# Performance work log

Hardware: AMD Instinct MI355X
Metric: run time of the kernel (lower is better)

## Reference

```python
import jax, jax.numpy as jnp
import numpy as np

NUM_CLASSES = 81
THRESH_HI = 0.5
THRESH_LO = 0.4
GAMMA = 2.0
ALPHA = 0.25
VARIANCE = (0.1, 0.2)  # cfg['variance'] in ssd.pytorch
B, P, T = 32, 24564, 20


def setup_inputs() -> dict:
    key = jax.random.key(0)
    k1, k2, k3, k4, k5, k6, k7 = jax.random.split(key, 7)
    loc_data = jax.random.normal(k1, (B, P, 4), jnp.float32)
    conf_data = jax.random.normal(k2, (B, P, NUM_CLASSES), jnp.float32)
    # priors in center form (cx, cy, w, h), all in [0,1]
    pcxy = jax.random.uniform(k3, (P, 2), minval=0.05, maxval=0.95)
    pwh = jax.random.uniform(k4, (P, 2), minval=0.04, maxval=0.5)
    priors = jnp.concatenate([pcxy, pwh], axis=-1).astype(jnp.float32)
    # ground-truth boxes in point form (xmin, ymin, xmax, ymax) + label
    tcxy = jax.random.uniform(k5, (B, T, 2), minval=0.1, maxval=0.9)
    twh = jax.random.uniform(k6, (B, T, 2), minval=0.05, maxval=0.4)
    boxes = jnp.clip(jnp.concatenate([tcxy - twh / 2, tcxy + twh / 2], -1), 0.0, 1.0)
    labels = jax.random.randint(k7, (B, T), 0, NUM_CLASSES - 1).astype(jnp.float32)
    targets = jnp.concatenate([boxes, labels[..., None]], axis=-1)  # [B,T,5]
    return {"loc_data": loc_data, "conf_data": conf_data, "priors": priors, "targets": targets}


def point_form(pr):
    # center form -> (xmin,ymin,xmax,ymax)
    return jnp.concatenate([pr[:, :2] - pr[:, 2:] / 2, pr[:, :2] + pr[:, 2:] / 2], -1)


def jaccard(box_a, box_b):
    # box_a [T,4], box_b [P,4], both point form -> IoU [T,P]
    lt = jnp.maximum(box_a[:, None, :2], box_b[None, :, :2])
    rb = jnp.minimum(box_a[:, None, 2:], box_b[None, :, 2:])
    wh = jnp.clip(rb - lt, 0.0)
    inter = wh[..., 0] * wh[..., 1]
    area_a = ((box_a[:, 2] - box_a[:, 0]) * (box_a[:, 3] - box_a[:, 1]))[:, None]
    area_b = ((box_b[:, 2] - box_b[:, 0]) * (box_b[:, 3] - box_b[:, 1]))[None, :]
    return inter / (area_a + area_b - inter)


def encode(matched, priors):
    # matched [P,4] point form, priors [P,4] center form
    g_cxcy = ((matched[:, :2] + matched[:, 2:]) / 2 - priors[:, :2]) / (VARIANCE[0] * priors[:, 2:])
    g_wh = jnp.log((matched[:, 2:] - matched[:, :2]) / priors[:, 2:]) / VARIANCE[1]
    return jnp.concatenate([g_cxcy, g_wh], -1)


def match_one(truths, labels, priors):
    # truths [T,4] point form, labels [T], priors [P,4] center form
    ov = jaccard(truths, point_form(priors))          # [T,P]
    best_prior_idx = jnp.argmax(ov, axis=1)           # [T] best prior per gt
    best_truth_overlap = jnp.max(ov, axis=0)          # [P]
    best_truth_idx = jnp.argmax(ov, axis=0)           # [P]
    # ensure every gt box keeps its best prior
    best_truth_overlap = best_truth_overlap.at[best_prior_idx].set(2.0)
    best_truth_idx = best_truth_idx.at[best_prior_idx].set(jnp.arange(truths.shape[0]))
    matched = truths[best_truth_idx]                  # [P,4]
    conf = labels[best_truth_idx].astype(jnp.int32) + 1
    conf = jnp.where(best_truth_overlap < THRESH_HI, -1, conf)  # ignore band
    conf = jnp.where(best_truth_overlap < THRESH_LO, 0, conf)   # background
    return encode(matched, priors), conf


def reference(loc_data, conf_data, priors, targets):
    truths = targets[..., :4]
    labels = targets[..., 4]
    loc_t, conf_t = jax.vmap(lambda t, l: match_one(t, l, priors))(truths, labels)
    pos = conf_t > 0                                  # [B,P]
    # smooth L1 over positive priors (sum reduction)
    diff = loc_data - loc_t
    ad = jnp.abs(diff)
    sl1 = jnp.where(ad < 1.0, 0.5 * diff * diff, ad - 0.5)
    loss_l = jnp.sum(sl1 * pos[..., None])
    # focal loss over ALL locations (ignore conf==-1)
    logits = conf_data.reshape(-1, NUM_CLASSES)
    tgt = conf_t.reshape(-1)
    valid = tgt >= 0
    tgt_safe = jnp.where(valid, tgt, 0)
    logpt = jnp.take_along_axis(jax.nn.log_softmax(logits, -1), tgt_safe[:, None], 1)[:, 0]
    pt = jnp.exp(logpt)
    alpha_t = jnp.where(tgt > 0, ALPHA, 1.0 - ALPHA)
    fl = -alpha_t * (1.0 - pt) ** GAMMA * logpt
    loss_c = jnp.sum(jnp.where(valid, fl, 0.0))
    n = jnp.sum(pos).astype(loc_data.dtype)
    return loss_l / n, loss_c / n
```

## Files before the change

kernel.cpp:

```cpp
#include <hip/hip_runtime.h>

#define NCLS 81
#define BB 32
#define PP 24564
#define TT 20
#define KM_BLOCKS_X 96
#define BP_SEGS 8
#define BP_SEG 3072
#define KL_BLOCKS 1792
#define KL_ROWS 32
#define KL_CHUNKS ((BB * PP) / KL_ROWS)
#define KL_F4 ((KL_ROWS * NCLS) / 4)

#define GLOAD_LDS16(g, l)                                                  \
    __builtin_amdgcn_global_load_lds(                                      \
        (const __attribute__((address_space(1))) void*)(g),                \
        (__attribute__((address_space(3))) void*)(l), 16, 0, 0)

__global__ __launch_bounds__(1024)
void k_bp(const float* __restrict__ priors,
          const float* __restrict__ targets,
          unsigned long long* __restrict__ bp_part)
{
    const int seg = blockIdx.x;
    const int b = blockIdx.y;

    __shared__ float trb[TT * 5];
    __shared__ unsigned long long wred[TT][16];
    if (threadIdx.x < TT * 5) trb[threadIdx.x] = targets[b * TT * 5 + threadIdx.x];
    __syncthreads();

    float X1[3], Y1[3], X2[3], Y2[3], pa[3];
    unsigned int pkey[3];
    bool ok[3];
    #pragma unroll
    for (int j = 0; j < 3; ++j) {
        int p = seg * BP_SEG + j * 1024 + threadIdx.x;
        ok[j] = p < PP;
        float4 pr = ok[j] ? ((const float4*)priors)[p] : make_float4(1.f, 1.f, 0.f, 0.f);
        float hw = __fmul_rn(pr.z, 0.5f), hh = __fmul_rn(pr.w, 0.5f);
        X1[j] = __fsub_rn(pr.x, hw); Y1[j] = __fsub_rn(pr.y, hh);
        X2[j] = __fadd_rn(pr.x, hw); Y2[j] = __fadd_rn(pr.y, hh);
        pa[j] = __fmul_rn(__fsub_rn(X2[j], X1[j]), __fsub_rn(Y2[j], Y1[j]));
        pkey[j] = 0xFFFFFFFFu - (unsigned)p;
    }

    const int wv = threadIdx.x >> 6;
    const int lane = threadIdx.x & 63;

    for (int t = 0; t < TT; ++t) {
        float tx1 = trb[t * 5 + 0], ty1 = trb[t * 5 + 1];
        float tx2 = trb[t * 5 + 2], ty2 = trb[t * 5 + 3];
        float ta = __fmul_rn(__fsub_rn(tx2, tx1), __fsub_rn(ty2, ty1));

        unsigned long long best = 0ull;
        #pragma unroll
        for (int j = 0; j < 3; ++j) {
            float lx = fmaxf(tx1, X1[j]), ly = fmaxf(ty1, Y1[j]);
            float rx = fminf(tx2, X2[j]), ry = fminf(ty2, Y2[j]);
            float w = fmaxf(__fsub_rn(rx, lx), 0.0f);
            float h = fmaxf(__fsub_rn(ry, ly), 0.0f);
            float inter = __fmul_rn(w, h);
            float denom = __fsub_rn(__fadd_rn(ta, pa[j]), inter);
            float ov = __fdiv_rn(inter, denom);
            unsigned long long key = ok[j]
                ? (((unsigned long long)__float_as_uint(ov) << 32) | pkey[j]) : 0ull;
            if (key > best) best = key;
        }
        #pragma unroll
        for (int s = 32; s; s >>= 1) {
            unsigned long long o = __shfl_xor(best, s, 64);
            if (o > best) best = o;
        }
        if (lane == 0) wred[t][wv] = best;
    }
    __syncthreads();
    if (threadIdx.x < TT) {
        unsigned long long m = wred[threadIdx.x][0];
        #pragma unroll
        for (int w = 1; w < 16; ++w) if (wred[threadIdx.x][w] > m) m = wred[threadIdx.x][w];
        bp_part[(b * TT + threadIdx.x) * BP_SEGS + seg] = m;
    }
}

__global__ __launch_bounds__(256)
void k_match(const float* __restrict__ loc,
             const float* __restrict__ priors,
             const float* __restrict__ targets,
             const unsigned long long* __restrict__ bp_part,
             unsigned char* __restrict__ code,
             float* __restrict__ pl, float* __restrict__ pn)
{
    const int b = blockIdx.y;
    const int p = blockIdx.x * 256 + threadIdx.x;

    __shared__ float trb[TT * 5];
    __shared__ unsigned int bpb[TT];
    if (threadIdx.x < TT * 5) trb[threadIdx.x] = targets[b * TT * 5 + threadIdx.x];
    if (threadIdx.x < TT) {
        const unsigned long long* q = bp_part + (b * TT + threadIdx.x) * BP_SEGS;
        unsigned long long m = q[0];
        #pragma unroll
        for (int s = 1; s < BP_SEGS; ++s) if (q[s] > m) m = q[s];
        bpb[threadIdx.x] = 0xFFFFFFFFu - (unsigned)(m & 0xFFFFFFFFull);
    }
    __syncthreads();

    float accL = 0.0f, accN = 0.0f;

    if (p < PP) {
        float px = priors[p * 4 + 0], py = priors[p * 4 + 1];
        float pw = priors[p * 4 + 2], ph = priors[p * 4 + 3];
        float hw = __fmul_rn(pw, 0.5f), hh = __fmul_rn(ph, 0.5f);
        float X1 = __fsub_rn(px, hw), Y1 = __fsub_rn(py, hh);
        float X2 = __fadd_rn(px, hw), Y2 = __fadd_rn(py, hh);
        float pa = __fmul_rn(__fsub_rn(X2, X1), __fsub_rn(Y2, Y1));

        float bI = -1.0f, bD = 1.0f;
        int bt = 0;
        #pragma unroll
        for (int t = 0; t < TT; ++t) {
            float tx1 = trb[t * 5 + 0], ty1 = trb[t * 5 + 1];
            float tx2 = trb[t * 5 + 2], ty2 = trb[t * 5 + 3];
            float ta2 = __fmul_rn(__fsub_rn(tx2, tx1), __fsub_rn(ty2, ty1));
            float lx = fmaxf(tx1, X1), ly = fmaxf(ty1, Y1);
            float rx = fminf(tx2, X2), ry = fminf(ty2, Y2);
            float w = fmaxf(__fsub_rn(rx, lx), 0.0f);
            float h = fmaxf(__fsub_rn(ry, ly), 0.0f);
            float inter = __fmul_rn(w, h);
            float denom = __fsub_rn(__fadd_rn(ta2, pa), inter);
            if (__fmul_rn(inter, bD) > __fmul_rn(bI, denom)) { bI = inter; bD = denom; bt = t; }
        }
        float bov = __fdiv_rn(bI, bD);

        bool forced = false;
        #pragma unroll
        for (int t = 0; t < TT; ++t) {
            if (bpb[t] == (unsigned)p) { bt = t; forced = true; }
        }
        if (forced) bov = 2.0f;

        int c = (int)trb[bt * 5 + 4] + 1;
        if (bov < 0.5f) c = -1;
        if (bov < 0.4f) c = 0;

        const int r = b * PP + p;
        code[r] = (unsigned char)(c + 1);

        if (c > 0) {
            float mx1 = trb[bt * 5 + 0], my1 = trb[bt * 5 + 1];
            float mx2 = trb[bt * 5 + 2], my2 = trb[bt * 5 + 3];
            float cx = __fmul_rn(__fadd_rn(mx1, mx2), 0.5f);
            float cy = __fmul_rn(__fadd_rn(my1, my2), 0.5f);
            float gx = __fdiv_rn(__fsub_rn(cx, px), __fmul_rn(0.1f, pw));
            float gy = __fdiv_rn(__fsub_rn(cy, py), __fmul_rn(0.1f, ph));
            float gw = __fdiv_rn(logf(__fdiv_rn(__fsub_rn(mx2, mx1), pw)), 0.2f);
            float gh = __fdiv_rn(logf(__fdiv_rn(__fsub_rn(my2, my1), ph)), 0.2f);
            const float* ld = loc + (size_t)r * 4;
            float g0 = ld[0] - gx, g1 = ld[1] - gy, g2 = ld[2] - gw, g3 = ld[3] - gh;
            float a0 = fabsf(g0), a1 = fabsf(g1), a2 = fabsf(g2), a3 = fabsf(g3);
            accL += (a0 < 1.0f) ? 0.5f * g0 * g0 : (a0 - 0.5f);
            accL += (a1 < 1.0f) ? 0.5f * g1 * g1 : (a1 - 0.5f);
            accL += (a2 < 1.0f) ? 0.5f * g2 * g2 : (a2 - 0.5f);
            accL += (a3 < 1.0f) ? 0.5f * g3 * g3 : (a3 - 0.5f);
            accN += 1.0f;
        }
    }

    __shared__ float red[256];
    red[threadIdx.x] = accL;
    __syncthreads();
    for (int s = 128; s; s >>= 1) {
        if (threadIdx.x < s) red[threadIdx.x] += red[threadIdx.x + s];
        __syncthreads();
    }
    if (threadIdx.x == 0) pl[blockIdx.y * KM_BLOCKS_X + blockIdx.x] = red[0];
    __syncthreads();

    red[threadIdx.x] = accN;
    __syncthreads();
    for (int s = 128; s; s >>= 1) {
        if (threadIdx.x < s) red[threadIdx.x] += red[threadIdx.x + s];
        __syncthreads();
    }
    if (threadIdx.x == 0) pn[blockIdx.y * KM_BLOCKS_X + blockIdx.x] = red[0];
}

__global__ __launch_bounds__(256)
void k_loss(const float* __restrict__ conf,
            const unsigned char* __restrict__ code,
            float* __restrict__ pc)
{
    __shared__ float buf[2][KL_ROWS * NCLS];

    const int tid = threadIdx.x;
    const int w = tid >> 6;
    const int lane = tid & 63;
    const int rl = tid >> 3;
    const int k = tid & 7;
    const float4* conf4 = (const float4*)conf;

    auto stage = [&](int c, int buf_idx) {
        const float4* src = conf4 + (size_t)c * KL_F4;
        float4* dst = (float4*)buf[buf_idx];
        #pragma unroll
        for (int j = 0; j < 2; ++j) {
            int idx = j * 256 + w * 64 + lane;
            GLOAD_LDS16(src + idx, dst + idx);
        }
        if (tid < KL_F4 - 512) {
            int idx = 512 + w * 64 + lane;
            GLOAD_LDS16(src + idx, dst + idx);
        }
    };

    const int c0 = blockIdx.x;
    stage(c0, 0);
    __syncthreads();

    float accC = 0.0f;
    int cur = 0;

    for (int c = c0; c < KL_CHUNKS; c += KL_BLOCKS) {
        int cn = c + KL_BLOCKS;
        if (cn < KL_CHUNKS) stage(cn, cur ^ 1);

        const float* row = buf[cur] + rl * NCLS;
        float se = 0.0f;
        #pragma unroll
        for (int i = 0; i < 10; ++i) se += __expf(row[k * 10 + i]);
        if (k == 0) se += __expf(row[80]);
        se += __shfl_xor(se, 1, 8);
        se += __shfl_xor(se, 2, 8);
        se += __shfl_xor(se, 4, 8);

        if (k == 0) {
            int r = c * KL_ROWS + rl;
            int cc = (int)code[r] - 1;
            if (cc >= 0) {
                float xt = row[cc];
                float logpt = xt - __logf(se);
                float pt = __expf(logpt);
                float at = (cc > 0) ? 0.25f : 0.75f;
                float om = 1.0f - pt;
                accC -= at * om * om * logpt;
            }
        }
        __syncthreads();
        cur ^= 1;
    }

    __shared__ float red[256];
    red[tid] = accC;
    __syncthreads();
    for (int s = 128; s; s >>= 1) {
        if (tid < s) red[tid] += red[tid + s];
        __syncthreads();
    }
    if (tid == 0) pc[blockIdx.x] = red[0];
}

__global__ __launch_bounds__(256)
void k_final(const float* __restrict__ pl, const float* __restrict__ pn,
             const float* __restrict__ pc, float* __restrict__ out)
{
    __shared__ float sl[256], sc[256], sn[256];
    float L = 0.0f, C = 0.0f, N = 0.0f;
    for (int i = threadIdx.x; i < BB * KM_BLOCKS_X; i += 256) { L += pl[i]; N += pn[i]; }
    for (int i = threadIdx.x; i < KL_BLOCKS; i += 256) C += pc[i];
    sl[threadIdx.x] = L; sc[threadIdx.x] = C; sn[threadIdx.x] = N;
    __syncthreads();
    for (int s = 128; s; s >>= 1) {
        if (threadIdx.x < s) {
            sl[threadIdx.x] += sl[threadIdx.x + s];
            sc[threadIdx.x] += sc[threadIdx.x + s];
            sn[threadIdx.x] += sn[threadIdx.x + s];
        }
        __syncthreads();
    }
    if (threadIdx.x == 0) {
        out[0] = sl[0] / sn[0];
        out[1] = sc[0] / sn[0];
    }
}

extern "C" void kernel_launch(void* const* d_in, const int* in_sizes, int n_in,
                              void* d_out, int out_size, void* d_ws, size_t ws_size,
                              hipStream_t stream)
{
    const float* loc     = (const float*)d_in[0];
    const float* conf    = (const float*)d_in[1];
    const float* priors  = (const float*)d_in[2];
    const float* targets = (const float*)d_in[3];
    float* out = (float*)d_out;

    char* ws = (char*)d_ws;
    unsigned long long* bp_part = (unsigned long long*)ws;
    unsigned char* code = (unsigned char*)(ws + 65536);
    float* pl = (float*)(ws + 65536 + 790528);
    float* pn = pl + BB * KM_BLOCKS_X;
    float* pc = pn + BB * KM_BLOCKS_X;

    k_bp<<<dim3(BP_SEGS, BB), 1024, 0, stream>>>(priors, targets, bp_part);
    k_match<<<dim3(KM_BLOCKS_X, BB), 256, 0, stream>>>(loc, priors, targets, bp_part, code, pl, pn);
    k_loss<<<KL_BLOCKS, 256, 0, stream>>>(conf, code, pc);
    k_final<<<1, 256, 0, stream>>>(pl, pn, pc, out);
}
```

Baseline: 85.32 us.

## Fuse prior matching into focal-loss kernel, dropping the code buffer and one launch

Merges the per-prior matching and smooth-L1 kernel into the conf-streaming focal-loss kernel. Each row's match is now computed inline by the k==0 lane, using targets and best-prior metadata that are double-buffered in LDS per chunk. This removes the intermediate byte code array round-trip and one kernel launch, and adds occupancy hints. The cost is that only one thread in eight does the 20-target IoU loop, which serialises compute inside a kernel that was mostly bandwidth-bound and may expose latency.

Measured after the change: 151.4 us. 1.77x slower.

```diff
diff --git a/kernel.cpp b/kernel.cpp
--- a/kernel.cpp
+++ b/kernel.cpp
@@ -4,7 +4,6 @@
 #define BB 32
 #define PP 24564
 #define TT 20
-#define KM_BLOCKS_X 96
 #define BP_SEGS 8
 #define BP_SEG 3072
 #define KL_BLOCKS 1792
@@ -83,115 +82,17 @@
     }
 }
 
-__global__ __launch_bounds__(256)
-void k_match(const float* __restrict__ loc,
-             const float* __restrict__ priors,
-             const float* __restrict__ targets,
-             const unsigned long long* __restrict__ bp_part,
-             unsigned char* __restrict__ code,
-             float* __restrict__ pl, float* __restrict__ pn)
-{
-    const int b = blockIdx.y;
-    const int p = blockIdx.x * 256 + threadIdx.x;
-
-    __shared__ float trb[TT * 5];
-    __shared__ unsigned int bpb[TT];
-    if (threadIdx.x < TT * 5) trb[threadIdx.x] = targets[b * TT * 5 + threadIdx.x];
-    if (threadIdx.x < TT) {
-        const unsigned long long* q = bp_part + (b * TT + threadIdx.x) * BP_SEGS;
-        unsigned long long m = q[0];
-        #pragma unroll
-        for (int s = 1; s < BP_SEGS; ++s) if (q[s] > m) m = q[s];
-        bpb[threadIdx.x] = 0xFFFFFFFFu - (unsigned)(m & 0xFFFFFFFFull);
-    }
-    __syncthreads();
-
-    float accL = 0.0f, accN = 0.0f;
-
-    if (p < PP) {
-        float px = priors[p * 4 + 0], py = priors[p * 4 + 1];
-        float pw = priors[p * 4 + 2], ph = priors[p * 4 + 3];
-        float hw = __fmul_rn(pw, 0.5f), hh = __fmul_rn(ph, 0.5f);
-        float X1 = __fsub_rn(px, hw), Y1 = __fsub_rn(py, hh);
-        float X2 = __fadd_rn(px, hw), Y2 = __fadd_rn(py, hh);
-        float pa = __fmul_rn(__fsub_rn(X2, X1), __fsub_rn(Y2, Y1));
-
-        float bI = -1.0f, bD = 1.0f;
-        int bt = 0;
-        #pragma unroll
-        for (int t = 0; t < TT; ++t) {
-            float tx1 = trb[t * 5 + 0], ty1 = trb[t * 5 + 1];
-            float tx2 = trb[t * 5 + 2], ty2 = trb[t * 5 + 3];
-            float ta2 = __fmul_rn(__fsub_rn(tx2, tx1), __fsub_rn(ty2, ty1));
-            float lx = fmaxf(tx1, X1), ly = fmaxf(ty1, Y1);
-            float rx = fminf(tx2, X2), ry = fminf(ty2, Y2);
-            float w = fmaxf(__fsub_rn(rx, lx), 0.0f);
-            float h = fmaxf(__fsub_rn(ry, ly), 0.0f);
-            float inter = __fmul_rn(w, h);
-            float denom = __fsub_rn(__fadd_rn(ta2, pa), inter);
-            if (__fmul_rn(inter, bD) > __fmul_rn(bI, denom)) { bI = inter; bD = denom; bt = t; }
-        }
-        float bov = __fdiv_rn(bI, bD);
-
-        bool forced = false;
-        #pragma unroll
-        for (int t = 0; t < TT; ++t) {
-            if (bpb[t] == (unsigned)p) { bt = t; forced = true; }
-        }
-        if (forced) bov = 2.0f;
-
-        int c = (int)trb[bt * 5 + 4] + 1;
-        if (bov < 0.5f) c = -1;
-        if (bov < 0.4f) c = 0;
-
-        const int r = b * PP + p;
-        code[r] = (unsigned char)(c + 1);
-
-        if (c > 0) {
-            float mx1 = trb[bt * 5 + 0], my1 = trb[bt * 5 + 1];
-            float mx2 = trb[bt * 5 + 2], my2 = trb[bt * 5 + 3];
-            float cx = __fmul_rn(__fadd_rn(mx1, mx2), 0.5f);
-            float cy = __fmul_rn(__fadd_rn(my1, my2), 0.5f);
-            float gx = __fdiv_rn(__fsub_rn(cx, px), __fmul_rn(0.1f, pw));
-            float gy = __fdiv_rn(__fsub_rn(cy, py), __fmul_rn(0.1f, ph));
-            float gw = __fdiv_rn(logf(__fdiv_rn(__fsub_rn(mx2, mx1), pw)), 0.2f);
-            float gh = __fdiv_rn(logf(__fdiv_rn(__fsub_rn(my2, my1), ph)), 0.2f);
-            const float* ld = loc + (size_t)r * 4;
-            float g0 = ld[0] - gx, g1 = ld[1] - gy, g2 = ld[2] - gw, g3 = ld[3] - gh;
-            float a0 = fabsf(g0), a1 = fabsf(g1), a2 = fabsf(g2), a3 = fabsf(g3);
-            accL += (a0 < 1.0f) ? 0.5f * g0 * g0 : (a0 - 0.5f);
-            accL += (a1 < 1.0f) ? 0.5f * g1 * g1 : (a1 - 0.5f);
-            accL += (a2 < 1.0f) ? 0.5f * g2 * g2 : (a2 - 0.5f);
-            accL += (a3 < 1.0f) ? 0.5f * g3 * g3 : (a3 - 0.5f);
-            accN += 1.0f;
-        }
-    }
-
-    __shared__ float red[256];
-    red[threadIdx.x] = accL;
-    __syncthreads();
-    for (int s = 128; s; s >>= 1) {
-        if (threadIdx.x < s) red[threadIdx.x] += red[threadIdx.x + s];
-        __syncthreads();
-    }
-    if (threadIdx.x == 0) pl[blockIdx.y * KM_BLOCKS_X + blockIdx.x] = red[0];
-    __syncthreads();
-
-    red[threadIdx.x] = accN;
-    __syncthreads();
-    for (int s = 128; s; s >>= 1) {
-        if (threadIdx.x < s) red[threadIdx.x] += red[threadIdx.x + s];
-        __syncthreads();
-    }
-    if (threadIdx.x == 0) pn[blockIdx.y * KM_BLOCKS_X + blockIdx.x] = red[0];
-}
-
-__global__ __launch_bounds__(256)
-void k_loss(const float* __restrict__ conf,
-            const unsigned char* __restrict__ code,
-            float* __restrict__ pc)
+__global__ __launch_bounds__(256, 4)
+void k_main(const float* __restrict__ conf,
+            const float* __restrict__ loc,
+            const float* __restrict__ priors,
+            const float* __restrict__ targets,
+            const unsigned long long* __restrict__ bp_part,
+            float* __restrict__ pl, float* __restrict__ pn, float* __restrict__ pc)
 {
     __shared__ float buf[2][KL_ROWS * NCLS];
+    __shared__ float trbS[2][2][TT * 5];
+    __shared__ unsigned int bpbS[2][2][TT];
 
     const int tid = threadIdx.x;
     const int w = tid >> 6;
@@ -200,30 +101,56 @@
     const int k = tid & 7;
     const float4* conf4 = (const float4*)conf;
 
-    auto stage = [&](int c, int buf_idx) {
+    auto stage = [&](int c, int bi) {
         const float4* src = conf4 + (size_t)c * KL_F4;
-        float4* dst = (float4*)buf[buf_idx];
+        float4* dst = (float4*)buf[bi];
         #pragma unroll
         for (int j = 0; j < 2; ++j) {
             int idx = j * 256 + w * 64 + lane;
             GLOAD_LDS16(src + idx, dst + idx);
         }
         if (tid < KL_F4 - 512) {
-            int idx = 512 + w * 64 + lane;
+            int idx = 512 + tid;
             GLOAD_LDS16(src + idx, dst + idx);
+        }
+    };
+
+    auto load_meta = [&](int c, int bi) {
+        int r0 = c * KL_ROWS;
+        int b0 = r0 / PP;
+        int b1 = (r0 + KL_ROWS - 1) / PP;
+        if (tid < 200) {
+            int which = tid / 100;
+            int i = tid - which * 100;
+            int bb = which ? b1 : b0;
+            trbS[bi][which][i] = targets[bb * 100 + i];
+        } else if (tid < 240) {
+            int q2 = tid - 200;
+            int which = q2 / 20;
+            int t = q2 - which * 20;
+            int bb = which ? b1 : b0;
+            const unsigned long long* q = bp_part + (bb * TT + t) * BP_SEGS;
+            unsigned long long m = q[0];
+            #pragma unroll
+            for (int s = 1; s < BP_SEGS; ++s) if (q[s] > m) m = q[s];
+            bpbS[bi][which][t] = 0xFFFFFFFFu - (unsigned)(m & 0xFFFFFFFFull);
         }
     };
 
     const int c0 = blockIdx.x;
     stage(c0, 0);
-    __syncthreads();
-
-    float accC = 0.0f;
+    load_meta(c0, 0);
+    __syncthreads();
+
+    float accL = 0.0f, accN = 0.0f, accC = 0.0f;
     int cur = 0;
 
     for (int c = c0; c < KL_CHUNKS; c += KL_BLOCKS) {
         int cn = c + KL_BLOCKS;
-        if (cn < KL_CHUNKS) stage(cn, cur ^ 1);
+        if (cn < KL_CHUNKS) {
+            stage(cn, cur ^ 1);
+            load_meta(cn, cur ^ 1);
+        }
 
         const float* row = buf[cur] + rl * NCLS;
         float se = 0.0f;
@@ -236,7 +163,66 @@
 
         if (k == 0) {
             int r = c * KL_ROWS + rl;
-            int cc = (int)code[r] - 1;
+            int b0 = (c * KL_ROWS) / PP;
+            int sel = (r >= (b0 + 1) * PP) ? 1 : 0;
+            int b = b0 + sel;
+            int p = r - b * PP;
+            const float* trb = &trbS[cur][sel][0];
+            const unsigned int* bpb = &bpbS[cur][sel][0];
+
+            float px = priors[p * 4 + 0], py = priors[p * 4 + 1];
+            float pw = priors[p * 4 + 2], ph = priors[p * 4 + 3];
+            float hw = __fmul_rn(pw, 0.5f), hh = __fmul_rn(ph, 0.5f);
+            float X1 = __fsub_rn(px, hw), Y1 = __fsub_rn(py, hh);
+            float X2 = __fadd_rn(px, hw), Y2 = __fadd_rn(py, hh);
+            float pa = __fmul_rn(__fsub_rn(X2, X1), __fsub_rn(Y2, Y1));
+
+            float bI = -1.0f, bD = 1.0f;
+            int bt = 0;
+            #pragma unroll
+            for (int t = 0; t < TT; ++t) {
+                float tx1 = trb[t * 5 + 0], ty1 = trb[t * 5 + 1];
+                float tx2 = trb[t * 5 + 2], ty2 = trb[t * 5 + 3];
+                float ta2 = __fmul_rn(__fsub_rn(tx2, tx1), __fsub_rn(ty2, ty1));
+                float lx = fmaxf(tx1, X1), ly = fmaxf(ty1, Y1);
+                float rx = fminf(tx2, X2), ry = fminf(ty2, Y2);
+                float ww = fmaxf(__fsub_rn(rx, lx), 0.0f);
+                float hh2 = fmaxf(__fsub_rn(ry, ly), 0.0f);
+                float inter = __fmul_rn(ww, hh2);
+                float denom = __fsub_rn(__fadd_rn(ta2, pa), inter);
+                if (__fmul_rn(inter, bD) > __fmul_rn(bI, denom)) { bI = inter; bD = denom; bt = t; }
+            }
+            float bov = __fdiv_rn(bI, bD);
+
+            bool forced = false;
+            #pragma unroll
+            for (int t = 0; t < TT; ++t) {
+                if (bpb[t] == (unsigned)p) { bt = t; forced = true; }
+            }
+            if (forced) bov = 2.0f;
+
+            int cc = (int)trb[bt * 5 + 4] + 1;
+            if (bov < 0.5f) cc = -1;
+            if (bov < 0.4f) cc = 0;
+
+            if (cc > 0) {
+                float mx1 = trb[bt * 5 + 0], my1 = trb[bt * 5 + 1];
+                float mx2 = trb[bt * 5 + 2], my2 = trb[bt * 5 + 3];
+                float cx = __fmul_rn(__fadd_rn(mx1, mx2), 0.5f);
+                float cy = __fmul_rn(__fadd_rn(my1, my2), 0.5f);
+                float gx = __fdiv_rn(__fsub_rn(cx, px), __fmul_rn(0.1f, pw));
+                float gy = __fdiv_rn(__fsub_rn(cy, py), __fmul_rn(0.1f, ph));
+                float gw = __fdiv_rn(logf(__fdiv_rn(__fsub_rn(mx2, mx1), pw)), 0.2f);
+                float gh = __fdiv_rn(logf(__fdiv_rn(__fsub_rn(my2, my1), ph)), 0.2f);
+                float4 ld = *(const float4*)(loc + (size_t)r * 4);
+                float g0 = ld.x - gx, g1 = ld.y - gy, g2 = ld.z - gw, g3 = ld.w - gh;
+                float a0 = fabsf(g0), a1 = fabsf(g1), a2 = fabsf(g2), a3 = fabsf(g3);
+                accL += (a0 < 1.0f) ? 0.5f * g0 * g0 : (a0 - 0.5f);
+                accL += (a1 < 1.0f) ? 0.5f * g1 * g1 : (a1 - 0.5f);
+                accL += (a2 < 1.0f) ? 0.5f * g2 * g2 : (a2 - 0.5f);
+                accL += (a3 < 1.0f) ? 0.5f * g3 * g3 : (a3 - 0.5f);
+                accN += 1.0f;
+            }
             if (cc >= 0) {
                 float xt = row[cc];
                 float logpt = xt - __logf(se);
@@ -251,6 +237,24 @@
     }
 
     __shared__ float red[256];
+    red[tid] = accL;
+    __syncthreads();
+    for (int s = 128; s; s >>= 1) {
+        if (tid < s) red[tid] += red[tid + s];
+        __syncthreads();
+    }
+    if (tid == 0) pl[blockIdx.x] = red[0];
+    __syncthreads();
+
+    red[tid] = accN;
+    __syncthreads();
+    for (int s = 128; s; s >>= 1) {
+        if (tid < s) red[tid] += red[tid + s];
+        __syncthreads();
+    }
+    if (tid == 0) pn[blockIdx.x] = red[0];
+    __syncthreads();
+
     red[tid] = accC;
     __syncthreads();
     for (int s = 128; s; s >>= 1) {
@@ -266,8 +270,9 @@
 {
     __shared__ float sl[256], sc[256], sn[256];
     float L = 0.0f, C = 0.0f, N = 0.0f;
-    for (int i = threadIdx.x; i < BB * KM_BLOCKS_X; i += 256) { L += pl[i]; N += pn[i]; }
-    for (int i = threadIdx.x; i < KL_BLOCKS; i += 256) C += pc[i];
+    for (int i = threadIdx.x; i < KL_BLOCKS; i += 256) {
+        L += pl[i]; N += pn[i]; C += pc[i];
+    }
     sl[threadIdx.x] = L; sc[threadIdx.x] = C; sn[threadIdx.x] = N;
     __syncthreads();
     for (int s = 128; s; s >>= 1) {
@@ -296,13 +301,11 @@
 
     char* ws = (char*)d_ws;
     unsigned long long* bp_part = (unsigned long long*)ws;
-    unsigned char* code = (unsigned char*)(ws + 65536);
-    float* pl = (float*)(ws + 65536 + 790528);
-    float* pn = pl + BB * KM_BLOCKS_X;
-    float* pc = pn + BB * KM_BLOCKS_X;
+    float* pl = (float*)(ws + 65536);
+    float* pn = pl + KL_BLOCKS;
+    float* pc = pn + KL_BLOCKS;
 
     k_bp<<<dim3(BP_SEGS, BB), 1024, 0, stream>>>(priors, targets, bp_part);
-    k_match<<<dim3(KM_BLOCKS_X, BB), 256, 0, stream>>>(loc, priors, targets, bp_part, code, pl, pn);
-    k_loss<<<KL_BLOCKS, 256, 0, stream>>>(conf, code, pc);
+    k_main<<<KL_BLOCKS, 256, 0, stream>>>(conf, loc, priors, targets, bp_part, pl, pn, pc);
     k_final<<<1, 256, 0, stream>>>(pl, pn, pc, out);
 }
```
